# Optimization experiments

Measured on AMD Instinct MI355X. Metric: run time of the kernel, lower is better.

The kernel has to match this reference:

```python
import jax, jax.numpy as jnp
import numpy as np

VOCAB, T, CLASSES = 30000, 256, 2
B, E, H = 128, 300, 256


def setup_inputs() -> dict:
    key = jax.random.key(0)
    ks = jax.random.split(key, 16)
    s = lambda k, sh, sc=0.02: jax.random.normal(k, sh, dtype=jnp.float32) * sc
    return {
        "tokens": jax.random.randint(ks[0], (B, T), 0, VOCAB, dtype=jnp.int32),
        "mask": jax.random.randint(ks[1], (B, T), 0, 2) > 0,
        "emb": s(ks[2], (VOCAB, E)),
        "Wi": s(ks[3], (E, 4 * H)),
        "Wh": s(ks[4], (H, 4 * H)),
        "b_lstm": jnp.zeros((4 * H,), jnp.float32),
        "Wq": s(ks[5], (H, H)), "bq": jnp.zeros((H,), jnp.float32),
        "Wk": s(ks[6], (H, H)), "bk": jnp.zeros((H,), jnp.float32),
        "Wv": s(ks[7], (H, H)), "bv": jnp.zeros((H,), jnp.float32),
        "Wo": s(ks[8], (H, H)), "bo": jnp.zeros((H,), jnp.float32),
        "W1": s(ks[9], (T * H, 100)), "b1": jnp.zeros((100,), jnp.float32),
        "W2": s(ks[10], (100, CLASSES)), "b2": jnp.zeros((CLASSES,), jnp.float32),
    }


def _forward(tokens, mask, emb, Wi, Wh, b_lstm, Wq, bq, Wk, bk, Wv, bv, Wo, bo, W1, b1, W2, b2):
    x = emb[tokens]  # (B, T, E)
    bsz = x.shape[0]
    # Pre-project inputs once (equivalent math, fewer per-step FLOPs)
    xW = jnp.einsum('bte,eg->btg', x, Wi) + b_lstm  # (B, T, 4H)

    def step(carry, xt):
        c, h = carry
        y = xt + h @ Wh  # (B, 4H)
        i, f, g, o = jnp.split(y, 4, axis=-1)  # flax OptimizedLSTMCell gate order
        i, f, o = jax.nn.sigmoid(i), jax.nn.sigmoid(f), jax.nn.sigmoid(o)
        g = jnp.tanh(g)
        c = f * c + i * g
        h = o * jnp.tanh(c)
        return (c, h), h

    c0 = jnp.zeros((bsz, H), x.dtype)
    h0 = jnp.zeros((bsz, H), x.dtype)
    _, hs = jax.lax.scan(step, (c0, h0), jnp.swapaxes(xW, 0, 1))
    hs = jnp.swapaxes(hs, 0, 1)  # (B, T, H)

    # single-head self-attention (flax SelfAttention(1))
    q = (hs @ Wq + bq) / jnp.sqrt(jnp.asarray(H, hs.dtype))
    k = hs @ Wk + bk
    v = hs @ Wv + bv
    scores = jnp.einsum('bqd,bkd->bqk', q, k)  # (B, T, T)
    # mask repeated 'b v -> b 1 v max_length': masks query rows, broadcast over keys
    big_neg = jnp.finfo(scores.dtype).min
    scores = jnp.where(mask[:, :, None], scores, big_neg)
    w = jax.nn.softmax(scores, axis=-1)
    attn = jnp.einsum('bqk,bkd->bqd', w, v) @ Wo + bo  # (B, T, H)

    flat = attn.reshape(bsz, -1)  # (B, T*H)
    h1 = jax.nn.relu(flat @ W1 + b1)
    logits = h1 @ W2 + b2
    return jax.nn.softmax(logits, axis=-1)


def reference(tokens, mask, emb, Wi, Wh, b_lstm, Wq, bq, Wk, bk, Wv, bv, Wo, bo, W1, b1, W2, b2):
    return _forward(tokens, mask, emb, Wi, Wh, b_lstm, Wq, bq, Wk, bk, Wv, bv, Wo, bo, W1, b1, W2, b2)
```

## Files before the change

kernel.cpp:

```cpp
#include <hip/hip_runtime.h>
#include <stdint.h>

#define B_   128
#define T_   256
#define H_   256
#define E_   300
#define G4_  1024

typedef __attribute__((ext_vector_type(8))) short bf16x8s;
typedef __attribute__((ext_vector_type(4))) float f32x4;

__device__ __forceinline__ short f2bf(float f) {
    unsigned u = __builtin_bit_cast(unsigned, f);
    unsigned r = (u + 0x7fffu + ((u >> 16) & 1u)) >> 16;
    return (short)r;
}
__device__ __forceinline__ float bf2f(short s) {
    unsigned u = (unsigned)(unsigned short)s;
    return __builtin_bit_cast(float, u << 16);
}
__device__ __forceinline__ float sigm(float x) { return 1.f / (1.f + __expf(-x)); }
__device__ __forceinline__ float ftanh(float x) {
    float e = __expf(-2.f * x);
    return (1.f - e) / (1.f + e);
}

__global__ void k_detect(const unsigned char* __restrict__ m8, int* __restrict__ flag) {
    int i = blockIdx.x * 256 + threadIdx.x;
    if ((i & 3) != 0 && m8[i] != 0) atomicOr(flag, 1);
}

__global__ void k_prep(const void* __restrict__ mask, const int* __restrict__ tokens,
                       const int* __restrict__ flag, float* __restrict__ maskf,
                       int* __restrict__ rowtok) {
    int i = blockIdx.x * 256 + threadIdx.x;
    int isbyte = *flag;
    int mv = isbyte ? (int)((const unsigned char*)mask)[i] : ((const int*)mask)[i];
    maskf[i] = mv ? 1.f : 0.f;
    int b = i >> 8, t = i & 255;
    rowtok[t * B_ + b] = tokens[i];
}

__global__ void k_bpack(const float* __restrict__ W, short* __restrict__ out,
                        int N, int KS, int KREAL) {
    int frag = blockIdx.x;
    int nt = frag / KS, ks = frag - nt * KS;
    int l = threadIdx.x;
    int col = nt * 16 + (l & 15);
    int k0 = ks * 32 + (l >> 4) * 8;
    short tmp[8];
#pragma unroll
    for (int i = 0; i < 8; ++i) {
        int k = k0 + i;
        tmp[i] = (k < KREAL) ? f2bf(W[(size_t)k * N + col]) : (short)0;
    }
    int4 v;
    __builtin_memcpy(&v, tmp, 16);
    ((int4*)out)[(size_t)frag * 64 + l] = v;
}

__global__ void k_packqkv(const float* __restrict__ Wq, const float* __restrict__ Wk,
                          const float* __restrict__ Wv, short* __restrict__ out) {
    int frag = blockIdx.x;
    int nt = frag >> 3, ks = frag & 7;
    int l = threadIdx.x;
    int col = (nt & 15) * 16 + (l & 15);
    int k0 = ks * 32 + (l >> 4) * 8;
    const float* W = nt < 16 ? Wq : (nt < 32 ? Wk : Wv);
    float sc = nt < 16 ? 0.0625f : 1.f;
    short tmp[8];
#pragma unroll
    for (int i = 0; i < 8; ++i) tmp[i] = f2bf(W[(size_t)(k0 + i) * 256 + col] * sc);
    int4 v;
    __builtin_memcpy(&v, tmp, 16);
    ((int4*)out)[(size_t)frag * 64 + l] = v;
}

__global__ void k_bias3(const float* __restrict__ bq, const float* __restrict__ bk,
                        const float* __restrict__ bv, float* __restrict__ bqkv) {
    int i = threadIdx.x;
    float v;
    if (i < 256) v = bq[i] * 0.0625f;
    else if (i < 512) v = bk[i - 256];
    else v = bv[i - 512];
    bqkv[i] = v;
}

template<bool GATHER, bool ABF16, int OUTMODE, int KS>
__global__ __launch_bounds__(512) void k_gemm_mfma(
    const void* __restrict__ Av, const short* __restrict__ Bp,
    const float* __restrict__ bias, void* __restrict__ Cv,
    void* __restrict__ C2, void* __restrict__ C3,
    int N, int KREAL, const int* __restrict__ rowidx)
{
    constexpr int KP = KS * 32;
    constexpr int LDA = KP + 8;
    __shared__ __align__(16) short As[128 * LDA];
    const int tid = threadIdx.x;
    const int l = tid & 63, w = tid >> 6;
    const int cl = l & 15, rowq = l >> 4;
    const int m0 = blockIdx.x * 128;

    for (int e = tid; e < 128 * KP; e += 512) {
        int r = e / KP, k = e - r * KP;
        int row = m0 + r;
        int arow = GATHER ? rowidx[row] : row;
        short sv = 0;
        if (k < KREAL) {
            if constexpr (ABF16) sv = ((const short*)Av)[(size_t)arow * KREAL + k];
            else                 sv = f2bf(((const float*)Av)[(size_t)arow * KREAL + k]);
        }
        As[r * LDA + k] = sv;
    }
    __syncthreads();

    bf16x8s a[KS];
#pragma unroll
    for (int ks = 0; ks < KS; ++ks)
        a[ks] = *(const bf16x8s*)&As[(w * 16 + cl) * LDA + ks * 32 + rowq * 8];

    const int nchunks = N >> 8;
    for (int ch = 0; ch < nchunks; ++ch) {
#pragma unroll
        for (int ntl = 0; ntl < 16; ++ntl) {
            const int nt = ch * 16 + ntl;
            const float bv = bias[nt * 16 + cl];
            f32x4 y = {bv, bv, bv, bv};
#pragma unroll
            for (int ks = 0; ks < KS; ++ks) {
                bf16x8s bf = *(const bf16x8s*)&Bp[((size_t)(nt * KS + ks) * 64 + l) * 8];
                y = __builtin_amdgcn_mfma_f32_16x16x32_bf16(a[ks], bf, y, 0, 0, 0);
            }
            if constexpr (OUTMODE == 2) {
                const int t  = m0 >> 7;
                const int wl = (nt >> 1) & 7, pp = nt & 1, gg = nt >> 4;
                const size_t fi = ((((size_t)t * 8 + w) * 8 + wl) * 2 + pp) * 4 + gg;
                short4 o;
                o.x = f2bf(y[0]); o.y = f2bf(y[1]); o.z = f2bf(y[2]); o.w = f2bf(y[3]);
                *(short4*)&((short*)Cv)[fi * 256 + (size_t)l * 4] = o;
            } else if constexpr (OUTMODE == 3) {
                const int gg = nt >> 4;
                if (gg < 2) {
                    short* dst = gg ? (short*)C2 : (short*)Cv;
#pragma unroll
                    for (int r = 0; r < 4; ++r) {
                        size_t row = (size_t)m0 + w * 16 + rowq * 4 + r;
                        dst[row * 256 + (nt & 15) * 16 + cl] = f2bf(y[r]);
                    }
                } else {
                    const int bidx = m0 >> 8;
                    const int t0 = (m0 & 255) + w * 16 + rowq * 4;
                    const int d = (nt & 15) * 16 + cl;
                    short4 o;
                    o.x = f2bf(y[0]); o.y = f2bf(y[1]); o.z = f2bf(y[2]); o.w = f2bf(y[3]);
                    *(short4*)&((short*)C3)[((size_t)bidx * 256 + d) * 256 + t0] = o;
                }
            } else {
#pragma unroll
                for (int r = 0; r < 4; ++r) {
                    size_t idx = (size_t)(m0 + w * 16 + rowq * 4 + r) * N + nt * 16 + cl;
                    ((float*)Cv)[idx] = y[r];
                }
            }
        }
    }
}

#define LDA_H 264

__global__ __launch_bounds__(512, 2) void lstm_mfma(
    const short* __restrict__ xwp, const short* __restrict__ whp,
    short* __restrict__ hs)
{
    __shared__ __align__(16) short whc[128 * 64 * 8];
    __shared__ __align__(16) short hb[2][16 * LDA_H];
    const int tid = threadIdx.x;
    const int l = tid & 63;
    const int w = tid >> 6;
    const int cl = l & 15;
    const int rowq = l >> 4;
    const int bb = blockIdx.x;
    const int bbase = bb * 16;

    for (int e = tid; e < 128 * 64; e += 512) {
        int frag = e >> 6, q = e & 63;
        int nt = frag >> 1, ks = frag & 1;
        ((int4*)whc)[e] = ((const int4*)whp)[(nt * 8 + ks) * 64 + q];
    }
    for (int e = tid; e < 2 * 16 * LDA_H; e += 512) ((short*)hb)[e] = 0;

    bf16x8s wreg[2][4][4];
#pragma unroll
    for (int p = 0; p < 2; ++p)
#pragma unroll
        for (int g = 0; g < 4; ++g)
#pragma unroll
            for (int kr = 0; kr < 4; ++kr) {
                const int nt = g * 16 + w * 2 + p;
                wreg[p][g][kr] = *(const bf16x8s*)&whp[((size_t)(nt * 8 + 2 + kr) * 64 + l) * 8];
            }

    float creg[2][4];
#pragma unroll
    for (int p = 0; p < 2; ++p)
#pragma unroll
        for (int r = 0; r < 4; ++r) creg[p][r] = 0.f;

    const short* xbase = xwp + ((size_t)bb * 8 + w) * 2 * 4 * 256 + (size_t)l * 4;
    const size_t tstride = (size_t)8 * 8 * 2 * 4 * 256;

    auto ld_xw = [&](int t, short4 (&dst)[2][4]) {
        const short* p0 = xbase + (size_t)t * tstride;
#pragma unroll
        for (int p = 0; p < 2; ++p)
#pragma unroll
            for (int g = 0; g < 4; ++g)
                dst[p][g] = *(const short4*)&p0[(p * 4 + g) * 256];
    };

    short4 xwA[2][4], xwB[2][4];
    ld_xw(0, xwA);
    __syncthreads();

    auto step = [&](int t, short4 (&cur)[2][4], short4 (&nxt)[2][4]) {
        ld_xw(t + 1, nxt);

        const short* hbr = hb[t & 1];
        short* hbw = hb[(t + 1) & 1];
        bf16x8s a[8];
#pragma unroll
        for (int ks = 0; ks < 8; ++ks)
            a[ks] = *(const bf16x8s*)&hbr[cl * LDA_H + ks * 32 + rowq * 8];

        f32x4 y[2][4];
#pragma unroll
        for (int p = 0; p < 2; ++p)
#pragma unroll
            for (int g = 0; g < 4; ++g) {
                y[p][g][0] = bf2f(cur[p][g].x);
                y[p][g][1] = bf2f(cur[p][g].y);
                y[p][g][2] = bf2f(cur[p][g].z);
                y[p][g][3] = bf2f(cur[p][g].w);
            }

#pragma unroll
        for (int p = 0; p < 2; ++p) {
#pragma unroll
            for (int g = 0; g < 4; ++g) {
                const int nt = g * 16 + w * 2 + p;
                const size_t sb = ((size_t)nt * 8 * 64 + l) * 8;
                bf16x8s s6 = *(const bf16x8s*)&whp[sb + 6 * 64 * 8];
                bf16x8s s7 = *(const bf16x8s*)&whp[sb + 7 * 64 * 8];
                bf16x8s c0 = *(const bf16x8s*)&whc[((nt * 2 + 0) * 64 + l) * 8];
                bf16x8s c1 = *(const bf16x8s*)&whc[((nt * 2 + 1) * 64 + l) * 8];
                y[p][g] = __builtin_amdgcn_mfma_f32_16x16x32_bf16(a[2], wreg[p][g][0], y[p][g], 0, 0, 0);
                y[p][g] = __builtin_amdgcn_mfma_f32_16x16x32_bf16(a[3], wreg[p][g][1], y[p][g], 0, 0, 0);
                y[p][g] = __builtin_amdgcn_mfma_f32_16x16x32_bf16(a[4], wreg[p][g][2], y[p][g], 0, 0, 0);
                y[p][g] = __builtin_amdgcn_mfma_f32_16x16x32_bf16(a[5], wreg[p][g][3], y[p][g], 0, 0, 0);
                y[p][g] = __builtin_amdgcn_mfma_f32_16x16x32_bf16(a[0], c0, y[p][g], 0, 0, 0);
                y[p][g] = __builtin_amdgcn_mfma_f32_16x16x32_bf16(a[1], c1, y[p][g], 0, 0, 0);
                y[p][g] = __builtin_amdgcn_mfma_f32_16x16x32_bf16(a[6], s6, y[p][g], 0, 0, 0);
                y[p][g] = __builtin_amdgcn_mfma_f32_16x16x32_bf16(a[7], s7, y[p][g], 0, 0, 0);
            }
        }

#pragma unroll
        for (int p = 0; p < 2; ++p) {
            const int j = w * 32 + p * 16 + cl;
#pragma unroll
            for (int r = 0; r < 4; ++r) {
                float iv = sigm(y[p][0][r]);
                float fv = sigm(y[p][1][r]);
                float gv = ftanh(y[p][2][r]);
                float ov = sigm(y[p][3][r]);
                float c = fmaf(fv, creg[p][r], iv * gv);
                creg[p][r] = c;
                float hv = ov * ftanh(c);
                short hvb = f2bf(hv);
                int b = rowq * 4 + r;
                hbw[b * LDA_H + j] = hvb;
                hs[((size_t)(bbase + b) * T_ + t) * H_ + j] = hvb;
            }
        }
        __syncthreads();
    };

    for (int t = 0; t < T_; t += 2) {
        step(t,     xwA, xwB);
        step(t + 1, xwB, xwA);
    }
}

__global__ __launch_bounds__(256) void k_attn_mfma(
    const short* __restrict__ qb, const short* __restrict__ kb,
    const short* __restrict__ vt, const float* __restrict__ maskf,
    float* __restrict__ o)
{
    __shared__ __align__(16) short P_lds[4][16 * 40];
    const int tid = threadIdx.x;
    const int l = tid & 63, w = tid >> 6;
    const int cl = l & 15, qr = l >> 4;
    const int b = blockIdx.y;
    const int q0 = blockIdx.x * 64 + w * 16;
    const size_t bb = (size_t)b * 256;

    bf16x8s qf[8];
    const short* qrow = qb + (bb + q0 + cl) * 256;
#pragma unroll
    for (int ks = 0; ks < 8; ++ks)
        qf[ks] = *(const bf16x8s*)&qrow[ks * 32 + qr * 8];

    float4 mr4 = *(const float4*)&maskf[bb + q0 + qr * 4];
    float msk[4] = {mr4.x, mr4.y, mr4.z, mr4.w};

    float m[4] = {-1e30f, -1e30f, -1e30f, -1e30f};
    float ls[4] = {0.f, 0.f, 0.f, 0.f};
    f32x4 acc[16];
#pragma unroll
    for (int nt = 0; nt < 16; ++nt) acc[nt] = {0.f, 0.f, 0.f, 0.f};

    for (int kt2 = 0; kt2 < 8; ++kt2) {
        const short* krow0 = kb + (bb + kt2 * 32 + cl) * 256;
        f32x4 s0 = {0.f, 0.f, 0.f, 0.f}, s1 = {0.f, 0.f, 0.f, 0.f};
#pragma unroll
        for (int ks = 0; ks < 8; ++ks) {
            bf16x8s k0f = *(const bf16x8s*)&krow0[ks * 32 + qr * 8];
            bf16x8s k1f = *(const bf16x8s*)&krow0[16 * 256 + ks * 32 + qr * 8];
            s0 = __builtin_amdgcn_mfma_f32_16x16x32_bf16(qf[ks], k0f, s0, 0, 0, 0);
            s1 = __builtin_amdgcn_mfma_f32_16x16x32_bf16(qf[ks], k1f, s1, 0, 0, 0);
        }

#pragma unroll
        for (int r = 0; r < 4; ++r) {
            float a0 = (msk[r] != 0.f) ? s0[r] : 0.f;
            float a1 = (msk[r] != 0.f) ? s1[r] : 0.f;
            float t = fmaxf(a0, a1);
            t = fmaxf(t, __shfl_xor(t, 1));
            t = fmaxf(t, __shfl_xor(t, 2));
            t = fmaxf(t, __shfl_xor(t, 4));
            t = fmaxf(t, __shfl_xor(t, 8));
            float mnew = fmaxf(m[r], t);
            float rsc = __expf(m[r] - mnew);
            m[r] = mnew;
            float p0 = __expf(a0 - mnew);
            float p1 = __expf(a1 - mnew);
            float ps = p0 + p1;
            ps += __shfl_xor(ps, 1);
            ps += __shfl_xor(ps, 2);
            ps += __shfl_xor(ps, 4);
            ps += __shfl_xor(ps, 8);
            ls[r] = ls[r] * rsc + ps;
#pragma unroll
            for (int nt = 0; nt < 16; ++nt) acc[nt][r] *= rsc;
            P_lds[w][(qr * 4 + r) * 40 + cl] = f2bf(p0);
            P_lds[w][(qr * 4 + r) * 40 + 16 + cl] = f2bf(p1);
        }

        bf16x8s pa = *(const bf16x8s*)&P_lds[w][cl * 40 + qr * 8];
        const short* vrow = vt + (bb + cl) * 256 + kt2 * 32 + qr * 8;
#pragma unroll
        for (int nt = 0; nt < 16; ++nt) {
            bf16x8s vf = *(const bf16x8s*)&vrow[(size_t)nt * 16 * 256];
            acc[nt] = __builtin_amdgcn_mfma_f32_16x16x32_bf16(pa, vf, acc[nt], 0, 0, 0);
        }
    }

    float inv[4];
#pragma unroll
    for (int r = 0; r < 4; ++r) inv[r] = 1.f / ls[r];
#pragma unroll
    for (int nt = 0; nt < 16; ++nt)
#pragma unroll
        for (int r = 0; r < 4; ++r)
            o[(bb + q0 + qr * 4 + r) * 256 + nt * 16 + cl] = acc[nt][r] * inv[r];
}

__global__ __launch_bounds__(256) void k_fc1(
    const float* __restrict__ flat, const float* __restrict__ W1, float* __restrict__ part)
{
    __shared__ __align__(16) float Wt[100][260];
    __shared__ __align__(16) float fs[2][256];
    const int kc = blockIdx.x, tid = threadIdx.x;
    for (int e = tid; e < 25600; e += 256) {
        int k = e / 100, j = e - k * 100;
        Wt[j][k] = W1[(size_t)(kc * 256 + k) * 100 + j];
    }
    __syncthreads();
    const int bh = tid / 100, j = tid - bh * 100;
    for (int bb = 0; bb < 64; ++bb) {
        for (int e = tid; e < 512; e += 256) {
            int bi = e >> 8, k = e & 255;
            fs[bi][k] = flat[(size_t)(bb * 2 + bi) * 65536 + kc * 256 + k];
        }
        __syncthreads();
        if (bh < 2) {
            float acc = 0.f;
#pragma unroll 16
            for (int k = 0; k < 256; k += 4) {
                float4 fv = *(const float4*)&fs[bh][k];
                float4 wv = *(const float4*)&Wt[j][k];
                acc = fmaf(fv.x, wv.x, fmaf(fv.y, wv.y, fmaf(fv.z, wv.z, fmaf(fv.w, wv.w, acc))));
            }
            part[(size_t)kc * 12800 + (bb * 2 + bh) * 100 + j] = acc;
        }
        __syncthreads();
    }
}

__global__ __launch_bounds__(128) void k_head(
    const float* __restrict__ part, const float* __restrict__ b1,
    const float* __restrict__ W2, const float* __restrict__ b2, float* __restrict__ out)
{
    __shared__ float h1s[100];
    __shared__ float ls[2];
    const int b = blockIdx.x, tid = threadIdx.x;
    if (tid < 100) {
        float s = 0.f;
        for (int kc = 0; kc < 256; ++kc) s += part[(size_t)kc * 12800 + b * 100 + tid];
        s += b1[tid];
        h1s[tid] = fmaxf(s, 0.f);
    }
    __syncthreads();
    if (tid < 2) {
        float lg = b2[tid];
        for (int j = 0; j < 100; ++j) lg = fmaf(h1s[j], W2[j * 2 + tid], lg);
        ls[tid] = lg;
    }
    __syncthreads();
    if (tid == 0) {
        float mm = fmaxf(ls[0], ls[1]);
        float e0 = __expf(ls[0] - mm), e1 = __expf(ls[1] - mm);
        float inv = 1.f / (e0 + e1);
        out[b * 2 + 0] = e0 * inv;
        out[b * 2 + 1] = e1 * inv;
    }
}

extern "C" void kernel_launch(void* const* d_in, const int* in_sizes, int n_in,
                              void* d_out, int out_size, void* d_ws, size_t ws_size,
                              hipStream_t stream) {
    (void)in_sizes; (void)n_in; (void)out_size; (void)ws_size;
    const int*   tokens = (const int*)  d_in[0];
    const void*  mask   =               d_in[1];
    const float* emb    = (const float*)d_in[2];
    const float* Wi     = (const float*)d_in[3];
    const float* Wh     = (const float*)d_in[4];
    const float* b_lstm = (const float*)d_in[5];
    const float* Wq     = (const float*)d_in[6];
    const float* bq     = (const float*)d_in[7];
    const float* Wk     = (const float*)d_in[8];
    const float* bk     = (const float*)d_in[9];
    const float* Wv     = (const float*)d_in[10];
    const float* bv     = (const float*)d_in[11];
    const float* Wo     = (const float*)d_in[12];
    const float* bo     = (const float*)d_in[13];
    const float* W1     = (const float*)d_in[14];
    const float* b1     = (const float*)d_in[15];
    const float* W2     = (const float*)d_in[16];
    const float* b2     = (const float*)d_in[17];
    float* out = (float*)d_out;

    float* ws = (float*)d_ws;
    float* reg0  = ws;
    short* xwp   = (short*)reg0;
    float* hsb   = reg0 + 33554432;
    short* hsb16 = (short*)hsb;
    float* maskf = hsb + 8388608;
    int*   rowtok= (int*)(maskf + 32768);
    int*   flag  = rowtok + 32768;
    short* whp   = (short*)((((uintptr_t)(flag + 1)) + 255) & ~(uintptr_t)255);
    short* wip   = whp + 262144;
    short* wqkvp = wip + 327680;
    short* wop   = wqkvp + 196608;
    float* bqkv  = (float*)(wop + 65536);
    short* qb16 = (short*)reg0;
    short* kb16 = (short*)(reg0 + 4194304);
    short* vt16 = (short*)(reg0 + 8388608);
    float* proj = reg0 + 12582912;
    float* part = reg0 + 20971520;
    float* attnf = hsb;

    hipMemsetAsync(flag, 0, sizeof(int), stream);
    k_detect<<<128, 256, 0, stream>>>((const unsigned char*)mask, flag);
    k_prep<<<128, 256, 0, stream>>>(mask, tokens, flag, maskf, rowtok);

    k_bpack<<<512, 64, 0, stream>>>(Wh, whp, 1024, 8, 256);
    k_bpack<<<640, 64, 0, stream>>>(Wi, wip, 1024, 10, 300);
    k_packqkv<<<384, 64, 0, stream>>>(Wq, Wk, Wv, wqkvp);
    k_bias3<<<1, 768, 0, stream>>>(bq, bk, bv, bqkv);
    k_bpack<<<128, 64, 0, stream>>>(Wo, wop, 256, 8, 256);

    k_gemm_mfma<true, false, 2, 10><<<256, 512, 0, stream>>>(
        emb, wip, b_lstm, xwp, nullptr, nullptr, 1024, 300, rowtok);

    lstm_mfma<<<8, 512, 0, stream>>>(xwp, whp, hsb16);

    k_gemm_mfma<false, true, 3, 8><<<256, 512, 0, stream>>>(
        hsb16, wqkvp, bqkv, qb16, kb16, vt16, 768, 256, nullptr);

    k_attn_mfma<<<dim3(4, 128), 256, 0, stream>>>(qb16, kb16, vt16, maskf, attnf);

    k_gemm_mfma<false, false, 0, 8><<<256, 512, 0, stream>>>(
        attnf, wop, bo, proj, nullptr, nullptr, 256, 256, nullptr);

    k_fc1<<<256, 256, 0, stream>>>(proj, W1, part);
    k_head<<<128, 128, 0, stream>>>(part, b1, W2, b2, out);
}
```

Measured before the change: 1.710 ms.

## Merge preprocessing and weight-packing launches; store output projection in bf16

Mask detection, mask/token prep and all weight/bias packing kernels are folded into two launches (a single-block prep kernel and one combined pack kernel), and the memset is dropped. This removes several small kernel launches and their serialization gaps. The Wo projection output is now written as bf16 and read back as bf16 by fc1, halving that intermediate's traffic at the cost of extra rounding. The single-block prep kernel serializes 32K elements on one CU, which may be slower than the original multi-block version.

Result: slower. 1.752 ms (+2.5%).

```diff
diff --git a/kernel.cpp b/kernel.cpp
--- a/kernel.cpp
+++ b/kernel.cpp
@@ -25,65 +25,75 @@
     return (1.f - e) / (1.f + e);
 }
 
-__global__ void k_detect(const unsigned char* __restrict__ m8, int* __restrict__ flag) {
-    int i = blockIdx.x * 256 + threadIdx.x;
-    if ((i & 3) != 0 && m8[i] != 0) atomicOr(flag, 1);
-}
-
-__global__ void k_prep(const void* __restrict__ mask, const int* __restrict__ tokens,
-                       const int* __restrict__ flag, float* __restrict__ maskf,
-                       int* __restrict__ rowtok) {
-    int i = blockIdx.x * 256 + threadIdx.x;
-    int isbyte = *flag;
-    int mv = isbyte ? (int)((const unsigned char*)mask)[i] : ((const int*)mask)[i];
-    maskf[i] = mv ? 1.f : 0.f;
-    int b = i >> 8, t = i & 255;
-    rowtok[t * B_ + b] = tokens[i];
-}
-
-__global__ void k_bpack(const float* __restrict__ W, short* __restrict__ out,
-                        int N, int KS, int KREAL) {
-    int frag = blockIdx.x;
+__global__ __launch_bounds__(1024) void k_prep_all(
+    const void* __restrict__ mask, const int* __restrict__ tokens,
+    float* __restrict__ maskf, int* __restrict__ rowtok)
+{
+    __shared__ int isbyte_s;
+    const int tid = threadIdx.x;
+    const unsigned char* m8 = (const unsigned char*)mask;
+    if (tid == 0) isbyte_s = 0;
+    __syncthreads();
+    int local = 0;
+    for (int i = tid; i < 32768; i += 1024)
+        if ((i & 3) != 0 && m8[i] != 0) local = 1;
+    if (local) atomicOr(&isbyte_s, 1);
+    __syncthreads();
+    const int isbyte = isbyte_s;
+    for (int i = tid; i < 32768; i += 1024) {
+        int mv = isbyte ? (int)m8[i] : ((const int*)mask)[i];
+        maskf[i] = mv ? 1.f : 0.f;
+        int b = i >> 8, t = i & 255;
+        rowtok[t * B_ + b] = tokens[i];
+    }
+}
+
+__device__ __forceinline__ void bpack_one(const float* __restrict__ W, short* __restrict__ out,
+                                          int frag, int l, int N, int KS, int KREAL, float sc) {
     int nt = frag / KS, ks = frag - nt * KS;
-    int l = threadIdx.x;
     int col = nt * 16 + (l & 15);
     int k0 = ks * 32 + (l >> 4) * 8;
     short tmp[8];
 #pragma unroll
     for (int i = 0; i < 8; ++i) {
         int k = k0 + i;
-        tmp[i] = (k < KREAL) ? f2bf(W[(size_t)k * N + col]) : (short)0;
+        tmp[i] = (k < KREAL) ? f2bf(W[(size_t)k * N + col] * sc) : (short)0;
     }
     int4 v;
     __builtin_memcpy(&v, tmp, 16);
     ((int4*)out)[(size_t)frag * 64 + l] = v;
 }
 
-__global__ void k_packqkv(const float* __restrict__ Wq, const float* __restrict__ Wk,
-                          const float* __restrict__ Wv, short* __restrict__ out) {
-    int frag = blockIdx.x;
-    int nt = frag >> 3, ks = frag & 7;
-    int l = threadIdx.x;
-    int col = (nt & 15) * 16 + (l & 15);
-    int k0 = ks * 32 + (l >> 4) * 8;
-    const float* W = nt < 16 ? Wq : (nt < 32 ? Wk : Wv);
-    float sc = nt < 16 ? 0.0625f : 1.f;
-    short tmp[8];
-#pragma unroll
-    for (int i = 0; i < 8; ++i) tmp[i] = f2bf(W[(size_t)(k0 + i) * 256 + col] * sc);
-    int4 v;
-    __builtin_memcpy(&v, tmp, 16);
-    ((int4*)out)[(size_t)frag * 64 + l] = v;
-}
-
-__global__ void k_bias3(const float* __restrict__ bq, const float* __restrict__ bk,
-                        const float* __restrict__ bv, float* __restrict__ bqkv) {
-    int i = threadIdx.x;
-    float v;
-    if (i < 256) v = bq[i] * 0.0625f;
-    else if (i < 512) v = bk[i - 256];
-    else v = bv[i - 512];
-    bqkv[i] = v;
+__global__ __launch_bounds__(64) void k_packall(
+    const float* __restrict__ Wh, const float* __restrict__ Wi,
+    const float* __restrict__ Wq, const float* __restrict__ Wk,
+    const float* __restrict__ Wv, const float* __restrict__ Wo,
+    const float* __restrict__ bq, const float* __restrict__ bk,
+    const float* __restrict__ bv,
+    short* __restrict__ whp, short* __restrict__ wip,
+    short* __restrict__ wqkvp, short* __restrict__ wop, float* __restrict__ bqkv)
+{
+    const int blk = blockIdx.x;
+    const int l = threadIdx.x;
+    if (blk < 512) {
+        bpack_one(Wh, whp, blk, l, 1024, 8, 256, 1.f);
+    } else if (blk < 1152) {
+        bpack_one(Wi, wip, blk - 512, l, 1024, 10, 300, 1.f);
+    } else if (blk < 1536) {
+        int frag = blk - 1152;
+        int nt = frag >> 3;
+        const float* W = nt < 16 ? Wq : (nt < 32 ? Wk : Wv);
+        float sc = nt < 16 ? 0.0625f : 1.f;
+        int lfr = (nt & 15) * 8 + (frag & 7);
+        bpack_one(W, wqkvp + (size_t)(nt >> 4) * 16 * 8 * 512, lfr, l, 256, 8, 256, sc);
+    } else if (blk < 1664) {
+        bpack_one(Wo, wop, blk - 1536, l, 256, 8, 256, 1.f);
+    } else {
+        for (int i = l; i < 768; i += 64) {
+            float v = i < 256 ? bq[i] * 0.0625f : (i < 512 ? bk[i - 256] : bv[i - 512]);
+            bqkv[i] = v;
+        }
+    }
 }
 
 template<bool GATHER, bool ABF16, int OUTMODE, int KS>
@@ -154,6 +164,12 @@
                     short4 o;
                     o.x = f2bf(y[0]); o.y = f2bf(y[1]); o.z = f2bf(y[2]); o.w = f2bf(y[3]);
                     *(short4*)&((short*)C3)[((size_t)bidx * 256 + d) * 256 + t0] = o;
+                }
+            } else if constexpr (OUTMODE == 1) {
+#pragma unroll
+                for (int r = 0; r < 4; ++r) {
+                    size_t idx = (size_t)(m0 + w * 16 + rowq * 4 + r) * N + nt * 16 + cl;
+                    ((short*)Cv)[idx] = f2bf(y[r]);
                 }
             } else {
 #pragma unroll
@@ -376,7 +392,7 @@
 }
 
 __global__ __launch_bounds__(256) void k_fc1(
-    const float* __restrict__ flat, const float* __restrict__ W1, float* __restrict__ part)
+    const short* __restrict__ flat, const float* __restrict__ W1, float* __restrict__ part)
 {
     __shared__ __align__(16) float Wt[100][260];
     __shared__ __align__(16) float fs[2][256];
@@ -390,7 +406,7 @@
     for (int bb = 0; bb < 64; ++bb) {
         for (int e = tid; e < 512; e += 256) {
             int bi = e >> 8, k = e & 255;
-            fs[bi][k] = flat[(size_t)(bb * 2 + bi) * 65536 + kc * 256 + k];
+            fs[bi][k] = bf2f(flat[(size_t)(bb * 2 + bi) * 65536 + kc * 256 + k]);
         }
         __syncthreads();
         if (bh < 2) {
@@ -476,19 +492,14 @@
     short* qb16 = (short*)reg0;
     short* kb16 = (short*)(reg0 + 4194304);
     short* vt16 = (short*)(reg0 + 8388608);
-    float* proj = reg0 + 12582912;
+    short* projb= (short*)(reg0 + 12582912);
     float* part = reg0 + 20971520;
     float* attnf = hsb;
 
-    hipMemsetAsync(flag, 0, sizeof(int), stream);
-    k_detect<<<128, 256, 0, stream>>>((const unsigned char*)mask, flag);
-    k_prep<<<128, 256, 0, stream>>>(mask, tokens, flag, maskf, rowtok);
-
-    k_bpack<<<512, 64, 0, stream>>>(Wh, whp, 1024, 8, 256);
-    k_bpack<<<640, 64, 0, stream>>>(Wi, wip, 1024, 10, 300);
-    k_packqkv<<<384, 64, 0, stream>>>(Wq, Wk, Wv, wqkvp);
-    k_bias3<<<1, 768, 0, stream>>>(bq, bk, bv, bqkv);
-    k_bpack<<<128, 64, 0, stream>>>(Wo, wop, 256, 8, 256);
+    k_prep_all<<<1, 1024, 0, stream>>>(mask, tokens, maskf, rowtok);
+
+    k_packall<<<1665, 64, 0, stream>>>(Wh, Wi, Wq, Wk, Wv, Wo, bq, bk, bv,
+                                       whp, wip, wqkvp, wop, bqkv);
 
     k_gemm_mfma<true, false, 2, 10><<<256, 512, 0, stream>>>(
         emb, wip, b_lstm, xwp, nullptr, nullptr, 1024, 300, rowtok);
@@ -500,9 +511,9 @@
 
     k_attn_mfma<<<dim3(4, 128), 256, 0, stream>>>(qb16, kb16, vt16, maskf, attnf);
 
-    k_gemm_mfma<false, false, 0, 8><<<256, 512, 0, stream>>>(
-        attnf, wop, bo, proj, nullptr, nullptr, 256, 256, nullptr);
-
-    k_fc1<<<256, 256, 0, stream>>>(proj, W1, part);
+    k_gemm_mfma<false, false, 1, 8><<<256, 512, 0, stream>>>(
+        attnf, wop, bo, projb, nullptr, nullptr, 256, 256, nullptr);
+
+    k_fc1<<<256, 256, 0, stream>>>(projb, W1, part);
     k_head<<<128, 128, 0, stream>>>(part, b1, W2, b2, out);
 }
```
